# Kernel tuning notes

Hardware: AMD Instinct MI355X
Metric: run time of the kernel (lower is better)

## Reference

```python
import jax, jax.numpy as jnp
import numpy as np

TOPK = 2
ROUTE_SCALE = 1.0


def setup_inputs() -> dict:
    key = jax.random.key(0)
    ks = jax.random.split(key, 9)
    B, T, C, E, H = 4, 2048, 1024, 8, 2752
    s = 0.02  # init scale for weights
    return {
        "x": jax.random.normal(ks[0], (B, T, C), dtype=jnp.float32),
        "gate_w": jax.random.normal(ks[1], (E, C), dtype=jnp.float32) * s,
        "expert_bias": jnp.zeros((E,), dtype=jnp.float32),
        "w1": jax.random.normal(ks[2], (E, C, H), dtype=jnp.float32) * s,
        "w2": jax.random.normal(ks[3], (E, H, C), dtype=jnp.float32) * s,
        "w3": jax.random.normal(ks[4], (E, C, H), dtype=jnp.float32) * s,
        "sw1": jax.random.normal(ks[5], (C, H), dtype=jnp.float32) * s,
        "sw2": jax.random.normal(ks[6], (H, C), dtype=jnp.float32) * s,
        "sw3": jax.random.normal(ks[7], (C, H), dtype=jnp.float32) * s,
    }


def reference(x, gate_w, expert_bias, w1, w2, w3, sw1, sw2, sw3):
    B, T, C = x.shape
    E = gate_w.shape[0]
    xf = x.reshape(-1, C)  # (N, C)
    N = xf.shape[0]

    # --- ExpertGate (sigmoid scoring, aux-loss-free, eval mode) ---
    scores = jax.nn.sigmoid(xf @ gate_w.T)            # (N, E), original scores
    routing = scores + expert_bias[None, :]           # bias only affects selection
    _, idx = jax.lax.top_k(routing, TOPK)             # (N, TOPK)
    w = jnp.take_along_axis(scores, idx, axis=1)      # gather original scores
    w = w / (w.sum(axis=-1, keepdims=True) + 1e-8)    # sigmoid normalization
    w = w * ROUTE_SCALE

    # Scatter top-k weights into a dense (N, E) combine matrix
    gates = jnp.zeros((N, E), dtype=xf.dtype)
    gates = gates.at[jnp.arange(N)[:, None], idx].add(w)

    # --- Routed SwiGLU experts (dense compute, gated combine) ---
    y = jnp.zeros_like(xf)
    for e in range(E):  # small fixed loop over experts
        h = jax.nn.silu(xf @ w1[e]) * (xf @ w3[e])    # (N, H)
        y = y + gates[:, e:e + 1] * (h @ w2[e])

    # --- Shared expert (always on) ---
    y = y + (jax.nn.silu(xf @ sw1) * (xf @ sw3)) @ sw2

    return y.reshape(B, T, C)
```

## Files before the change

kernel.cpp:

```cpp
#include <hip/hip_runtime.h>
#include <hip/hip_bf16.h>
#include <stdint.h>

#define E_ 8
#define C_ 1024
#define H_ 2752
#define NTOK 8192
#define CAP_ROWS 17408
#define ROUTED_XB 136
#define SHARED_XB 64
#define SHARED_HBASE 17408
#define HROWS 25600

typedef unsigned short u16;
typedef __attribute__((ext_vector_type(8))) short bf16x8;
typedef __attribute__((ext_vector_type(4))) float f32x4;

static constexpr size_t SZ_XB    = (size_t)NTOK * C_ * 2;
static constexpr size_t SZ_WT    = (size_t)E_ * H_ * C_ * 2;
static constexpr size_t SZ_SWT   = (size_t)H_ * C_ * 2;
static constexpr size_t SZ_H     = (size_t)HROWS * H_ * 2;

static constexpr size_t OFF_XB   = 0;
static constexpr size_t OFF_W1T  = OFF_XB   + SZ_XB;
static constexpr size_t OFF_W3T  = OFF_W1T  + SZ_WT;
static constexpr size_t OFF_W2T  = OFF_W3T  + SZ_WT;
static constexpr size_t OFF_SW1T = OFF_W2T  + SZ_WT;
static constexpr size_t OFF_SW3T = OFF_SW1T + SZ_SWT;
static constexpr size_t OFF_SW2T = OFF_SW3T + SZ_SWT;
static constexpr size_t OFF_H    = OFF_SW2T + SZ_SWT;
static constexpr size_t OFF_RIDX = OFF_H    + SZ_H;
static constexpr size_t OFF_RW   = OFF_RIDX + (size_t)NTOK*2*4;
static constexpr size_t OFF_OFFS = OFF_RW   + (size_t)NTOK*2*4;
static constexpr size_t OFF_PTOK = OFF_OFFS + 64;
static constexpr size_t OFF_PW   = OFF_PTOK + (size_t)CAP_ROWS*4;
static constexpr size_t WS_NEED  = OFF_PW   + (size_t)CAP_ROWS*4;

__device__ __forceinline__ u16 f2bf(float f) {
  union { float f; uint32_t u; } v; v.f = f;
  uint32_t r = v.u + 0x7FFFu + ((v.u >> 16) & 1u);
  return (u16)(r >> 16);
}

__device__ __forceinline__ void gld16(const void* g, void* l) {
  uint32_t lo = (uint32_t)(uintptr_t)l;
  lo = __builtin_amdgcn_readfirstlane(lo);
  __builtin_amdgcn_global_load_lds(
      (const __attribute__((address_space(1))) void*)g,
      (__attribute__((address_space(3))) void*)(uintptr_t)lo, 16, 0, 0);
}

#define MFMA16(A,B,C) __builtin_amdgcn_mfma_f32_16x16x32_bf16((A),(B),(C),0,0,0)

__global__ __launch_bounds__(256) void gate_kernel(
    const float* __restrict__ x, const float* __restrict__ gw,
    const float* __restrict__ bias, u16* __restrict__ xb,
    int* __restrict__ ridx, float* __restrict__ rw)
{
  const int n = blockIdx.x, t = threadIdx.x;
  const float4 v = *(const float4*)(x + (size_t)n * C_ + t * 4);
  union { u16 u[4]; uint2 d; } pk;
  pk.u[0] = f2bf(v.x); pk.u[1] = f2bf(v.y); pk.u[2] = f2bf(v.z); pk.u[3] = f2bf(v.w);
  *(uint2*)(xb + (size_t)n * C_ + t * 4) = pk.d;

  float p[E_];
#pragma unroll
  for (int e = 0; e < E_; ++e) {
    const float4 g = *(const float4*)(gw + (size_t)e * C_ + t * 4);
    p[e] = v.x * g.x + v.y * g.y + v.z * g.z + v.w * g.w;
  }
#pragma unroll
  for (int e = 0; e < E_; ++e)
    for (int off = 32; off > 0; off >>= 1) p[e] += __shfl_down(p[e], off);

  __shared__ float red[4][E_];
  const int wv = t >> 6;
  if ((t & 63) == 0) {
#pragma unroll
    for (int e = 0; e < E_; ++e) red[wv][e] = p[e];
  }
  __syncthreads();
  if (t == 0) {
    float sc[E_], rt[E_];
#pragma unroll
    for (int e = 0; e < E_; ++e) {
      const float d = red[0][e] + red[1][e] + red[2][e] + red[3][e];
      const float s = 1.f / (1.f + expf(-d));
      sc[e] = s; rt[e] = s + bias[e];
    }
    int i0 = 0; float b0 = rt[0];
#pragma unroll
    for (int e = 1; e < E_; ++e) if (rt[e] > b0) { b0 = rt[e]; i0 = e; }
    int i1 = -1; float b1 = -1e30f;
#pragma unroll
    for (int e = 0; e < E_; ++e) if (e != i0 && rt[e] > b1) { b1 = rt[e]; i1 = e; }
    const float s0 = sc[i0], s1 = sc[i1];
    const float inv = 1.f / (s0 + s1 + 1e-8f);
    ridx[2 * n] = i0; ridx[2 * n + 1] = i1;
    rw[2 * n] = s0 * inv; rw[2 * n + 1] = s1 * inv;
  }
}

__global__ __launch_bounds__(256) void transpose_cs_kernel(
    const float* __restrict__ w1, const float* __restrict__ w3,
    const float* __restrict__ sw1, const float* __restrict__ sw3,
    u16* __restrict__ w1t, u16* __restrict__ w3t,
    u16* __restrict__ sw1t, u16* __restrict__ sw3t)
{
  const int z = blockIdx.z;
  const float* src; u16* dst;
  if      (z < 8)  { src = w1 + (size_t)z * C_ * H_;       dst = w1t + (size_t)z * H_ * C_; }
  else if (z < 16) { src = w3 + (size_t)(z - 8) * C_ * H_; dst = w3t + (size_t)(z - 8) * H_ * C_; }
  else if (z == 16){ src = sw1; dst = sw1t; }
  else             { src = sw3; dst = sw3t; }
  __shared__ float tile[32][33];
  const int tx = threadIdx.x, ty = threadIdx.y;
  const int s0 = blockIdx.x * 32;
  const int r0 = blockIdx.y * 32;
#pragma unroll
  for (int i = 0; i < 4; ++i)
    tile[ty + 8 * i][tx] = src[(size_t)(r0 + ty + 8 * i) * H_ + s0 + tx];
  __syncthreads();
#pragma unroll
  for (int i = 0; i < 4; ++i)
    dst[(size_t)(s0 + ty + 8 * i) * C_ + r0 + tx] = f2bf(tile[tx][ty + 8 * i]);
}

__global__ __launch_bounds__(256) void transpose_sc_kernel(
    const float* __restrict__ w2, const float* __restrict__ sw2,
    u16* __restrict__ w2t, u16* __restrict__ sw2t)
{
  const int z = blockIdx.z;
  const float* src; u16* dst;
  if (z < 8) { src = w2 + (size_t)z * H_ * C_; dst = w2t + (size_t)z * C_ * H_; }
  else       { src = sw2; dst = sw2t; }
  __shared__ float tile[32][33];
  const int tx = threadIdx.x, ty = threadIdx.y;
  const int s0 = blockIdx.x * 32;
  const int r0 = blockIdx.y * 32;
#pragma unroll
  for (int i = 0; i < 4; ++i)
    tile[ty + 8 * i][tx] = src[(size_t)(r0 + ty + 8 * i) * C_ + s0 + tx];
  __syncthreads();
#pragma unroll
  for (int i = 0; i < 4; ++i)
    dst[(size_t)(s0 + ty + 8 * i) * H_ + r0 + tx] = f2bf(tile[tx][ty + 8 * i]);
}

__global__ __launch_bounds__(256) void route_scan_kernel(
    const int* __restrict__ ridx, const float* __restrict__ rw,
    int* __restrict__ offsets, int* __restrict__ perm_tok, float* __restrict__ perm_w)
{
  __shared__ int cnt[256][E_];
  __shared__ int pref[E_][257];
  __shared__ int offs[E_ + 1];
  __shared__ int totals[E_];
  const int t = threadIdx.x;
#pragma unroll
  for (int e = 0; e < E_; ++e) cnt[t][e] = 0;
  for (int j = 0; j < 64; ++j) { const int e = ridx[t * 64 + j]; cnt[t][e]++; }
  __syncthreads();
  if (t < E_) {
    int run = 0;
    for (int i = 0; i < 256; ++i) { pref[t][i] = run; run += cnt[i][t]; }
    totals[t] = run; pref[t][256] = run;
  }
  __syncthreads();
  if (t == 0) {
    int o = 0;
    for (int e = 0; e < E_; ++e) { offs[e] = o; o += (totals[e] + 127) & ~127; }
    offs[E_] = o;
    for (int i = 0; i <= E_; ++i) offsets[i] = offs[i];
  }
  __syncthreads();
#pragma unroll
  for (int e = 0; e < E_; ++e) cnt[t][e] = offs[e] + pref[e][t];
  for (int j = 0; j < 64; ++j) {
    const int a = t * 64 + j;
    const int e = ridx[a];
    const int p = cnt[t][e]++;
    perm_tok[p] = a >> 1;
    perm_w[p] = rw[a];
  }
  __syncthreads();
  for (int e = 0; e < E_; ++e) {
    for (int p = offs[e] + totals[e] + t; p < offs[e + 1]; p += 256) {
      perm_tok[p] = 0; perm_w[p] = 0.f;
    }
  }
}

__global__ __launch_bounds__(256, 2) void gemm1_m(
    const u16* __restrict__ xb, const u16* __restrict__ w1t_all,
    const u16* __restrict__ w3t_all, const u16* __restrict__ sw1t,
    const u16* __restrict__ sw3t, u16* __restrict__ hbuf,
    const int* __restrict__ offsets, const int* __restrict__ ptok)
{
  __shared__ u16 lds[3 * 8192];
  const int t = threadIdx.x;
  const int bx = blockIdx.x;
  const int n0 = blockIdx.y * 128;

  const u16 *b1w, *b3w; int row0; size_t hr0; int gather;
  if (bx < ROUTED_XB) {
    row0 = bx * 128;
    if (row0 >= offsets[8]) return;
    int e = 0;
#pragma unroll
    for (int i = 0; i < 7; ++i) if (row0 >= offsets[i + 1]) e = i + 1;
    b1w = w1t_all + (size_t)e * (H_ * C_);
    b3w = w3t_all + (size_t)e * (H_ * C_);
    hr0 = (size_t)row0; gather = 1;
  } else {
    row0 = (bx - ROUTED_XB) * 128;
    b1w = sw1t; b3w = sw3t; hr0 = (size_t)SHARED_HBASE + row0; gather = 0;
  }

  const int tq = t >> 3;
  const int cb = (((t & 7) ^ (tq & 7)) << 4);
  const char* gA[4]; const char* gB1[4]; const char* gB3[4];
#pragma unroll
  for (int i = 0; i < 4; ++i) {
    const int m = i * 32 + tq;
    const int tok = gather ? ptok[row0 + m] : (row0 + m);
    gA[i] = (const char*)xb + (size_t)tok * (C_ * 2) + cb;
    int nn = n0 + m; if (nn > H_ - 1) nn = H_ - 1;
    gB1[i] = (const char*)b1w + (size_t)nn * (C_ * 2) + cb;
    gB3[i] = (const char*)b3w + (size_t)nn * (C_ * 2) + cb;
  }
  char* lwave = (char*)lds + (t >> 6) * 1024;

  f32x4 acc1[4][4], acc3[4][4];
#pragma unroll
  for (int i = 0; i < 4; ++i)
#pragma unroll
    for (int j = 0; j < 4; ++j) { acc1[i][j] = f32x4{0,0,0,0}; acc3[i][j] = f32x4{0,0,0,0}; }

  const int lane = t & 63;
  const int l15 = lane & 15, lhi = lane >> 4, swz = lane & 7;
  const int wm = (t >> 7) & 1, wn = (t >> 6) & 1;
  int arow[4], brow[4];
#pragma unroll
  for (int f = 0; f < 4; ++f) {
    arow[f] = (wm * 64 + f * 16 + l15) * 128;
    brow[f] = (wn * 64 + f * 16 + l15) * 128;
  }
  const char* ldsc = (const char*)lds;

  for (int kt = 0; kt < C_ / 64; ++kt) {
    const int kb = kt * 128;
#pragma unroll
    for (int i = 0; i < 4; ++i) gld16(gA[i]  + kb, lwave + i * 4096);
#pragma unroll
    for (int i = 0; i < 4; ++i) gld16(gB1[i] + kb, lwave + 16384 + i * 4096);
#pragma unroll
    for (int i = 0; i < 4; ++i) gld16(gB3[i] + kb, lwave + 32768 + i * 4096);
    __syncthreads();
#pragma unroll
    for (int kk = 0; kk < 2; ++kk) {
      const int co = ((((kk << 2) | lhi)) ^ swz) << 4;
      bf16x8 a[4], b1[4], b3[4];
#pragma unroll
      for (int f = 0; f < 4; ++f) a[f]  = *(const bf16x8*)(ldsc + arow[f] + co);
#pragma unroll
      for (int f = 0; f < 4; ++f) b1[f] = *(const bf16x8*)(ldsc + 16384 + brow[f] + co);
#pragma unroll
      for (int f = 0; f < 4; ++f) b3[f] = *(const bf16x8*)(ldsc + 32768 + brow[f] + co);
#pragma unroll
      for (int mf = 0; mf < 4; ++mf)
#pragma unroll
        for (int nf = 0; nf < 4; ++nf) {
          acc1[mf][nf] = MFMA16(a[mf], b1[nf], acc1[mf][nf]);
          acc3[mf][nf] = MFMA16(a[mf], b3[nf], acc3[mf][nf]);
        }
    }
    __syncthreads();
  }

  const int rbase = wm * 64 + lhi * 4;
  const int cbase = n0 + wn * 64 + l15;
#pragma unroll
  for (int mf = 0; mf < 4; ++mf)
#pragma unroll
    for (int q = 0; q < 4; ++q) {
      const int r = rbase + mf * 16 + q;
      u16* hrow = hbuf + (hr0 + r) * H_;
#pragma unroll
      for (int nf = 0; nf < 4; ++nf) {
        const int c = cbase + nf * 16;
        if (c < H_) {
          const float v1 = acc1[mf][nf][q], v3 = acc3[mf][nf][q];
          const float sv = v1 / (1.f + __expf(-v1));
          hrow[c] = f2bf(sv * v3);
        }
      }
    }
}

__global__ __launch_bounds__(256, 2) void gemm2_m(
    const u16* __restrict__ hbuf, const u16* __restrict__ w2t_all,
    const u16* __restrict__ sw2t, float* __restrict__ y,
    const int* __restrict__ offsets, const int* __restrict__ ptok,
    const float* __restrict__ pw)
{
  __shared__ u16 lds[2 * 8192];
  const int t = threadIdx.x;
  const int bx = blockIdx.x;
  const int n0 = blockIdx.y * 128;

  int row0; size_t hr0; const u16* bW; int routed;
  if (bx < ROUTED_XB) {
    row0 = bx * 128;
    if (row0 >= offsets[8]) return;
    int e = 0;
#pragma unroll
    for (int i = 0; i < 7; ++i) if (row0 >= offsets[i + 1]) e = i + 1;
    bW = w2t_all + (size_t)e * (C_ * H_);
    hr0 = (size_t)row0; routed = 1;
  } else {
    row0 = (bx - ROUTED_XB) * 128;
    bW = sw2t; hr0 = (size_t)SHARED_HBASE + row0; routed = 0;
  }

  const int tq = t >> 3;
  const int cb = (((t & 7) ^ (tq & 7)) << 4);
  const char* gA[4]; const char* gB[4];
#pragma unroll
  for (int i = 0; i < 4; ++i) {
    const int m = i * 32 + tq;
    gA[i] = (const char*)hbuf + (hr0 + m) * (size_t)(H_ * 2) + cb;
    gB[i] = (const char*)bW + (size_t)(n0 + m) * (H_ * 2) + cb;
  }
  char* lwave = (char*)lds + (t >> 6) * 1024;

  f32x4 acc[4][4];
#pragma unroll
  for (int i = 0; i < 4; ++i)
#pragma unroll
    for (int j = 0; j < 4; ++j) acc[i][j] = f32x4{0,0,0,0};

  const int lane = t & 63;
  const int l15 = lane & 15, lhi = lane >> 4, swz = lane & 7;
  const int wm = (t >> 7) & 1, wn = (t >> 6) & 1;
  int arow[4], brow[4];
#pragma unroll
  for (int f = 0; f < 4; ++f) {
    arow[f] = (wm * 64 + f * 16 + l15) * 128;
    brow[f] = (wn * 64 + f * 16 + l15) * 128;
  }
  const char* ldsc = (const char*)lds;

  for (int kt = 0; kt < 43; ++kt) {
    const int kb = kt * 128;
#pragma unroll
    for (int i = 0; i < 4; ++i) gld16(gA[i] + kb, lwave + i * 4096);
#pragma unroll
    for (int i = 0; i < 4; ++i) gld16(gB[i] + kb, lwave + 16384 + i * 4096);
    __syncthreads();
#pragma unroll
    for (int kk = 0; kk < 2; ++kk) {
      const int co = ((((kk << 2) | lhi)) ^ swz) << 4;
      bf16x8 a[4], b[4];
#pragma unroll
      for (int f = 0; f < 4; ++f) a[f] = *(const bf16x8*)(ldsc + arow[f] + co);
#pragma unroll
      for (int f = 0; f < 4; ++f) b[f] = *(const bf16x8*)(ldsc + 16384 + brow[f] + co);
#pragma unroll
      for (int mf = 0; mf < 4; ++mf)
#pragma unroll
        for (int nf = 0; nf < 4; ++nf)
          acc[mf][nf] = MFMA16(a[mf], b[nf], acc[mf][nf]);
    }
    __syncthreads();
  }

  const int rbase = wm * 64 + lhi * 4;
  const int cbase = n0 + wn * 64 + l15;
#pragma unroll
  for (int mf = 0; mf < 4; ++mf)
#pragma unroll
    for (int q = 0; q < 4; ++q) {
      const int hr = (int)hr0 + rbase + mf * 16 + q;
      const float wgt = routed ? pw[hr] : 1.0f;
      if (wgt != 0.f) {
        const int tok = routed ? ptok[hr] : (hr - SHARED_HBASE);
        float* yr = y + (size_t)tok * C_;
#pragma unroll
        for (int nf = 0; nf < 4; ++nf)
          atomicAdd(yr + cbase + nf * 16, wgt * acc[mf][nf][q]);
      }
    }
}

extern "C" void kernel_launch(void* const* d_in, const int* in_sizes, int n_in,
                              void* d_out, int out_size, void* d_ws, size_t ws_size,
                              hipStream_t stream)
{
  const float* x    = (const float*)d_in[0];
  const float* gw   = (const float*)d_in[1];
  const float* bias = (const float*)d_in[2];
  const float* w1   = (const float*)d_in[3];
  const float* w2   = (const float*)d_in[4];
  const float* w3   = (const float*)d_in[5];
  const float* sw1  = (const float*)d_in[6];
  const float* sw2  = (const float*)d_in[7];
  const float* sw3  = (const float*)d_in[8];
  float* y = (float*)d_out;
  char* ws = (char*)d_ws;
  if (ws_size < WS_NEED) return;

  u16*   xb    = (u16*)(ws + OFF_XB);
  u16*   w1t   = (u16*)(ws + OFF_W1T);
  u16*   w3t   = (u16*)(ws + OFF_W3T);
  u16*   w2t   = (u16*)(ws + OFF_W2T);
  u16*   sw1t  = (u16*)(ws + OFF_SW1T);
  u16*   sw3t  = (u16*)(ws + OFF_SW3T);
  u16*   sw2t  = (u16*)(ws + OFF_SW2T);
  u16*   hbuf  = (u16*)(ws + OFF_H);
  int*   ridx  = (int*)(ws + OFF_RIDX);
  float* rwt   = (float*)(ws + OFF_RW);
  int*   offs  = (int*)(ws + OFF_OFFS);
  int*   ptok  = (int*)(ws + OFF_PTOK);
  float* pw    = (float*)(ws + OFF_PW);

  hipMemsetAsync(y, 0, (size_t)out_size * 4, stream);
  gate_kernel<<<NTOK, 256, 0, stream>>>(x, gw, bias, xb, ridx, rwt);
  transpose_cs_kernel<<<dim3(H_ / 32, C_ / 32, 18), dim3(32, 8), 0, stream>>>(
      w1, w3, sw1, sw3, w1t, w3t, sw1t, sw3t);
  transpose_sc_kernel<<<dim3(C_ / 32, H_ / 32, 9), dim3(32, 8), 0, stream>>>(
      w2, sw2, w2t, sw2t);
  route_scan_kernel<<<1, 256, 0, stream>>>(ridx, rwt, offs, ptok, pw);

  gemm1_m<<<dim3(ROUTED_XB + SHARED_XB, 22), 256, 0, stream>>>(
      xb, w1t, w3t, sw1t, sw3t, hbuf, offs, ptok);
  gemm2_m<<<dim3(ROUTED_XB + SHARED_XB, 8), 256, 0, stream>>>(
      hbuf, w2t, sw2t, y, offs, ptok, pw);
}
```

Before: 695.4 us.

## Replace atomic scatter in second GEMM with bf16 staging and gather-combine kernel

The second GEMM now writes its unweighted results as bf16 rows into a staging buffer that reuses the w1t workspace region, instead of doing weighted fp32 atomicAdds into the output. A new combine kernel uses an inverse permutation built in route_scan to gather each token's shared and two routed rows, apply the gate weights and write y directly, which also removes the memset. Both GEMMs swap grid axes so the N tiles vary fastest, and launch-bounds occupancy hints are raised. This adds an extra kernel pass and bf16 rounding of partial outputs, and relies on w1t no longer being needed after gemm1.

```diff
diff --git a/kernel.cpp b/kernel.cpp
--- a/kernel.cpp
+++ b/kernel.cpp
@@ -34,12 +34,18 @@
 static constexpr size_t OFF_OFFS = OFF_RW   + (size_t)NTOK*2*4;
 static constexpr size_t OFF_PTOK = OFF_OFFS + 64;
 static constexpr size_t OFF_PW   = OFF_PTOK + (size_t)CAP_ROWS*4;
-static constexpr size_t WS_NEED  = OFF_PW   + (size_t)CAP_ROWS*4;
+static constexpr size_t OFF_INV  = OFF_PW   + (size_t)CAP_ROWS*4;
+static constexpr size_t WS_NEED  = OFF_INV  + (size_t)NTOK*2*4;
+
+static constexpr size_t OFF_OUT  = OFF_W1T;
 
 __device__ __forceinline__ u16 f2bf(float f) {
   union { float f; uint32_t u; } v; v.f = f;
   uint32_t r = v.u + 0x7FFFu + ((v.u >> 16) & 1u);
   return (u16)(r >> 16);
+}
+__device__ __forceinline__ float bfu(uint32_t v) {
+  union { uint32_t u; float f; } x; x.u = v << 16; return x.f;
 }
 
 __device__ __forceinline__ void gld16(const void* g, void* l) {
@@ -149,7 +155,8 @@
 
 __global__ __launch_bounds__(256) void route_scan_kernel(
     const int* __restrict__ ridx, const float* __restrict__ rw,
-    int* __restrict__ offsets, int* __restrict__ perm_tok, float* __restrict__ perm_w)
+    int* __restrict__ offsets, int* __restrict__ perm_tok,
+    float* __restrict__ perm_w, int* __restrict__ invp)
 {
   __shared__ int cnt[256][E_];
   __shared__ int pref[E_][257];
@@ -181,6 +188,7 @@
     const int p = cnt[t][e]++;
     perm_tok[p] = a >> 1;
     perm_w[p] = rw[a];
+    invp[a] = p;
   }
   __syncthreads();
   for (int e = 0; e < E_; ++e) {
@@ -190,7 +198,7 @@
   }
 }
 
-__global__ __launch_bounds__(256, 2) void gemm1_m(
+__global__ __launch_bounds__(256, 3) void gemm1_m(
     const u16* __restrict__ xb, const u16* __restrict__ w1t_all,
     const u16* __restrict__ w3t_all, const u16* __restrict__ sw1t,
     const u16* __restrict__ sw3t, u16* __restrict__ hbuf,
@@ -198,12 +206,12 @@
 {
   __shared__ u16 lds[3 * 8192];
   const int t = threadIdx.x;
-  const int bx = blockIdx.x;
-  const int n0 = blockIdx.y * 128;
+  const int n0 = blockIdx.x * 128;
+  const int by = blockIdx.y;
 
   const u16 *b1w, *b3w; int row0; size_t hr0; int gather;
-  if (bx < ROUTED_XB) {
-    row0 = bx * 128;
+  if (by < ROUTED_XB) {
+    row0 = by * 128;
     if (row0 >= offsets[8]) return;
     int e = 0;
 #pragma unroll
@@ -212,7 +220,7 @@
     b3w = w3t_all + (size_t)e * (H_ * C_);
     hr0 = (size_t)row0; gather = 1;
   } else {
-    row0 = (bx - ROUTED_XB) * 128;
+    row0 = (by - ROUTED_XB) * 128;
     b1w = sw1t; b3w = sw3t; hr0 = (size_t)SHARED_HBASE + row0; gather = 0;
   }
 
@@ -297,29 +305,28 @@
     }
 }
 
-__global__ __launch_bounds__(256, 2) void gemm2_m(
+__global__ __launch_bounds__(256, 4) void gemm2_m(
     const u16* __restrict__ hbuf, const u16* __restrict__ w2t_all,
-    const u16* __restrict__ sw2t, float* __restrict__ y,
-    const int* __restrict__ offsets, const int* __restrict__ ptok,
-    const float* __restrict__ pw)
+    const u16* __restrict__ sw2t, u16* __restrict__ outb,
+    const int* __restrict__ offsets)
 {
   __shared__ u16 lds[2 * 8192];
   const int t = threadIdx.x;
-  const int bx = blockIdx.x;
-  const int n0 = blockIdx.y * 128;
-
-  int row0; size_t hr0; const u16* bW; int routed;
-  if (bx < ROUTED_XB) {
-    row0 = bx * 128;
+  const int n0 = blockIdx.x * 128;
+  const int by = blockIdx.y;
+
+  int row0; size_t hr0; const u16* bW;
+  if (by < ROUTED_XB) {
+    row0 = by * 128;
     if (row0 >= offsets[8]) return;
     int e = 0;
 #pragma unroll
     for (int i = 0; i < 7; ++i) if (row0 >= offsets[i + 1]) e = i + 1;
     bW = w2t_all + (size_t)e * (C_ * H_);
-    hr0 = (size_t)row0; routed = 1;
+    hr0 = (size_t)row0;
   } else {
-    row0 = (bx - ROUTED_XB) * 128;
-    bW = sw2t; hr0 = (size_t)SHARED_HBASE + row0; routed = 0;
+    row0 = (by - ROUTED_XB) * 128;
+    bW = sw2t; hr0 = (size_t)SHARED_HBASE + row0;
   }
 
   const int tq = t >> 3;
@@ -380,16 +387,30 @@
   for (int mf = 0; mf < 4; ++mf)
 #pragma unroll
     for (int q = 0; q < 4; ++q) {
-      const int hr = (int)hr0 + rbase + mf * 16 + q;
-      const float wgt = routed ? pw[hr] : 1.0f;
-      if (wgt != 0.f) {
-        const int tok = routed ? ptok[hr] : (hr - SHARED_HBASE);
-        float* yr = y + (size_t)tok * C_;
-#pragma unroll
-        for (int nf = 0; nf < 4; ++nf)
-          atomicAdd(yr + cbase + nf * 16, wgt * acc[mf][nf][q]);
-      }
-    }
+      u16* orow = outb + (hr0 + rbase + mf * 16 + q) * C_;
+#pragma unroll
+      for (int nf = 0; nf < 4; ++nf)
+        orow[cbase + nf * 16] = f2bf(acc[mf][nf][q]);
+    }
+}
+
+__global__ __launch_bounds__(256) void combine_kernel(
+    const u16* __restrict__ outb, const int* __restrict__ invp,
+    const float* __restrict__ rw, float* __restrict__ y)
+{
+  const int n = blockIdx.x, t = threadIdx.x;
+  const int c4 = t * 4;
+  const int p0 = invp[2 * n], p1 = invp[2 * n + 1];
+  const float g0 = rw[2 * n], g1 = rw[2 * n + 1];
+  const uint2 s = *(const uint2*)(outb + ((size_t)SHARED_HBASE + n) * C_ + c4);
+  const uint2 a = *(const uint2*)(outb + (size_t)p0 * C_ + c4);
+  const uint2 b = *(const uint2*)(outb + (size_t)p1 * C_ + c4);
+  float4 o;
+  o.x = bfu(s.x & 0xffffu) + g0 * bfu(a.x & 0xffffu) + g1 * bfu(b.x & 0xffffu);
+  o.y = bfu(s.x >> 16)     + g0 * bfu(a.x >> 16)     + g1 * bfu(b.x >> 16);
+  o.z = bfu(s.y & 0xffffu) + g0 * bfu(a.y & 0xffffu) + g1 * bfu(b.y & 0xffffu);
+  o.w = bfu(s.y >> 16)     + g0 * bfu(a.y >> 16)     + g1 * bfu(b.y >> 16);
+  *(float4*)(y + (size_t)n * C_ + c4) = o;
 }
 
 extern "C" void kernel_launch(void* const* d_in, const int* in_sizes, int n_in,
@@ -417,22 +438,24 @@
   u16*   sw3t  = (u16*)(ws + OFF_SW3T);
   u16*   sw2t  = (u16*)(ws + OFF_SW2T);
   u16*   hbuf  = (u16*)(ws + OFF_H);
+  u16*   outb  = (u16*)(ws + OFF_OUT);
   int*   ridx  = (int*)(ws + OFF_RIDX);
   float* rwt   = (float*)(ws + OFF_RW);
   int*   offs  = (int*)(ws + OFF_OFFS);
   int*   ptok  = (int*)(ws + OFF_PTOK);
   float* pw    = (float*)(ws + OFF_PW);
-
-  hipMemsetAsync(y, 0, (size_t)out_size * 4, stream);
+  int*   invp  = (int*)(ws + OFF_INV);
+
   gate_kernel<<<NTOK, 256, 0, stream>>>(x, gw, bias, xb, ridx, rwt);
   transpose_cs_kernel<<<dim3(H_ / 32, C_ / 32, 18), dim3(32, 8), 0, stream>>>(
       w1, w3, sw1, sw3, w1t, w3t, sw1t, sw3t);
   transpose_sc_kernel<<<dim3(C_ / 32, H_ / 32, 9), dim3(32, 8), 0, stream>>>(
       w2, sw2, w2t, sw2t);
-  route_scan_kernel<<<1, 256, 0, stream>>>(ridx, rwt, offs, ptok, pw);
-
-  gemm1_m<<<dim3(ROUTED_XB + SHARED_XB, 22), 256, 0, stream>>>(
+  route_scan_kernel<<<1, 256, 0, stream>>>(ridx, rwt, offs, ptok, pw, invp);
+
+  gemm1_m<<<dim3(22, ROUTED_XB + SHARED_XB), 256, 0, stream>>>(
       xb, w1t, w3t, sw1t, sw3t, hbuf, offs, ptok);
-  gemm2_m<<<dim3(ROUTED_XB + SHARED_XB, 8), 256, 0, stream>>>(
-      hbuf, w2t, sw2t, y, offs, ptok, pw);
-}
+  gemm2_m<<<dim3(8, ROUTED_XB + SHARED_XB), 256, 0, stream>>>(
+      hbuf, w2t, sw2t, outb, offs);
+  combine_kernel<<<NTOK, 256, 0, stream>>>(outb, invp, rwt, y);
+}
```

After: 1.151 ms. 1.65x slower.
